# Kernel optimization log

Hardware: AMD Instinct MI355X
Metric: run time of the kernel (lower is better)

The kernel has to match this reference:

```python
import jax, jax.numpy as jnp
import numpy as np

B, T, F, D, O, L = 64, 512, 20, 1024, 1095, 3


def setup_inputs() -> dict:
    key = jax.random.key(0)
    ks = jax.random.split(key, 8)
    return {
        "x": jax.random.normal(ks[0], (B, T, F), jnp.float32),
        "c": jnp.zeros((L, B, D), jnp.float32),  # accepted but ignored, like the torch module
        "W1": jax.random.normal(ks[1], (F, D), jnp.float32) * 0.05,
        "b1": jnp.zeros((D,), jnp.float32),
        "sru_W": jax.random.normal(ks[2], (L, D, 3 * D), jnp.float32) * 0.02,
        "sru_v": jax.random.normal(ks[3], (L, 2, D), jnp.float32) * 0.1,  # v_f, v_r per layer
        "sru_b": jnp.zeros((L, 2, D), jnp.float32),  # b_f, b_r per layer
        "W3": jax.random.normal(ks[4], (D, O), jnp.float32) * 0.02,
        "b3": jnp.zeros((O,), jnp.float32),
    }


def _sru_layer(h, W, vf, vr, bf, br):
    # h: (t, b, d) time-major
    t, b, d = h.shape
    U = jnp.einsum('tbd,de->tbe', h, W).reshape(t, b, 3, d)

    def step(c_prev, inp):
        u0, u1, u2, xt = inp
        f = jax.nn.sigmoid(u1 + vf * c_prev + bf)
        c_new = f * c_prev + (1.0 - f) * u0
        r = jax.nn.sigmoid(u2 + vr * c_new + br)
        h_t = r * c_new + (1.0 - r) * xt  # highway, identity activation (sru default)
        return c_new, h_t

    c0 = jnp.zeros((b, d), h.dtype)
    c_fin, h_out = jax.lax.scan(step, c0, (U[:, :, 0], U[:, :, 1], U[:, :, 2], h))
    return h_out, c_fin


def reference(x, c, W1, b1, sru_W, sru_v, sru_b, W3, b3):
    b, t, f = x.shape
    h = (x.reshape(b * t, f) @ W1 + b1).reshape(b, t, -1)
    h = jnp.transpose(h, (1, 0, 2))  # (t, b, d) time-major
    c_fins = []
    for l in range(L):
        h, c_fin = _sru_layer(h, sru_W[l], sru_v[l, 0], sru_v[l, 1], sru_b[l, 0], sru_b[l, 1])
        c_fins.append(c_fin)
    h = jnp.transpose(h, (1, 0, 2)).reshape(b * t, -1)
    y = h @ W3 + b3  # (b*t, O)
    return y, jnp.stack(c_fins)
```

## Files before the change

### kernel.cpp

```cpp
#include <hip/hip_runtime.h>
#include <hip/hip_bf16.h>

#define B_ 64
#define T_ 512
#define F_ 20
#define D_ 1024
#define O_ 1095
#define L_ 3
#define OPAD 1280

typedef __attribute__((ext_vector_type(8))) short bf16x8;
typedef __attribute__((ext_vector_type(4))) float f32x4;

__device__ __forceinline__ void async16(const void* g, void* l) {
    __builtin_amdgcn_global_load_lds(
        (const __attribute__((address_space(1))) unsigned int*)g,
        (__attribute__((address_space(3))) unsigned int*)l, 16, 0, 0);
}

__global__ __launch_bounds__(256) void fc1_kernel(
    const float* __restrict__ x, const float* __restrict__ W1,
    const float* __restrict__ b1, __hip_bfloat16* __restrict__ h)
{
    __shared__ float xs[64][F_];
    const int tid = threadIdx.x;
    const int d4  = tid * 4;
    const int r0  = blockIdx.x * 64;
    const int t   = r0 >> 6;

    for (int i = tid; i < 64 * F_; i += 256) {
        int r = i / F_, f = i - r * F_;
        xs[r][f] = x[((size_t)r * T_ + t) * F_ + f];
    }

    float4 w[F_];
#pragma unroll
    for (int f = 0; f < F_; ++f)
        w[f] = *(const float4*)(W1 + (size_t)f * D_ + d4);
    float4 bias = *(const float4*)(b1 + d4);

    __syncthreads();

    for (int r = 0; r < 64; ++r) {
        float a0 = bias.x, a1 = bias.y, a2 = bias.z, a3 = bias.w;
#pragma unroll
        for (int f = 0; f < F_; ++f) {
            float xv = xs[r][f];
            a0 = fmaf(xv, w[f].x, a0);
            a1 = fmaf(xv, w[f].y, a1);
            a2 = fmaf(xv, w[f].z, a2);
            a3 = fmaf(xv, w[f].w, a3);
        }
        union { __hip_bfloat162 h2[2]; float2 f2; } o;
        o.h2[0] = __float22bfloat162_rn(float2{a0, a1});
        o.h2[1] = __float22bfloat162_rn(float2{a2, a3});
        *(float2*)(h + ((size_t)(r0 + r) << 10) + d4) = o.f2;
    }
}

__global__ __launch_bounds__(256) void transpose_cast(
    const float* __restrict__ in, __hip_bfloat16* __restrict__ out,
    int K, int N, int Npad)
{
    __shared__ float tile[32][33];
    int k0 = blockIdx.x * 32;
    int n0 = blockIdx.y * 32;
    int tx = threadIdx.x & 31, ty = threadIdx.x >> 5;
#pragma unroll
    for (int r = 0; r < 4; ++r) {
        int n = n0 + tx;
        int k = k0 + ty + r * 8;
        tile[ty + r * 8][tx] = (n < N) ? in[(size_t)k * N + n] : 0.f;
    }
    __syncthreads();
#pragma unroll
    for (int r = 0; r < 4; ++r) {
        int nn = n0 + ty + r * 8;
        out[(size_t)nn * K + k0 + tx] = __float2bfloat16(tile[tx][ty + r * 8]);
    }
}

template<bool GUARD_N, bool REMAP, bool OUT_BF16>
__global__ __launch_bounds__(512, 2) void gemm256(
    const __hip_bfloat16* __restrict__ A,
    const __hip_bfloat16* __restrict__ Bt,
    void* __restrict__ Cv,
    int ldc, int Nreal, const float* __restrict__ bias, int nTilesN)
{
    constexpr int K  = 1024;
    constexpr int NT = K / 64;

    __shared__ __align__(16) char smem[131072];
    char* As = smem;
    char* Bs = smem + 65536;

    const int tid  = threadIdx.x;
    const int lane = tid & 63;
    const int w    = tid >> 6;

    const int nwg = gridDim.x;
    const int q8 = nwg >> 3, r8 = nwg & 7;
    const int xcd = blockIdx.x & 7, loc = blockIdx.x >> 3;
    const int wgid = (xcd < r8 ? xcd * (q8 + 1)
                               : r8 * (q8 + 1) + (xcd - r8) * q8) + loc;
    const int by = wgid / nTilesN;
    const int bx = wgid - by * nTilesN;
    const int tileM = by * 256;
    const int tileN = bx * 256;

    const int wm = (w >> 2) * 128;
    const int wn = (w & 3) * 64;
    const int lr = lane & 15;
    const int kl = lane >> 4;
    const int sw = (lr & 7) << 4;

    const int srow = w * 8 + (lane >> 3);
    const int scol = ((lane & 7) ^ ((lane >> 3) & 7)) << 3;
    const __hip_bfloat16* pAs = A  + (size_t)(tileM + srow) * K + scol;
    const __hip_bfloat16* pBs = Bt + (size_t)(tileN + srow) * K + scol;
    const int ldsW = w * 1024;

    f32x4  acc[8][4] = {};
    bf16x8 a[4][2], b[4][2];

    auto stageA = [&](int kt, int h) {
        char* dst = As + ((kt & 1) << 15) + (h << 14) + ldsW;
        const __hip_bfloat16* src = pAs + (size_t)h * 128 * K + kt * 64;
        async16(src, dst);
        async16(src + 64 * K, dst + 8192);
    };
    auto stageB = [&](int kt, int h) {
        char* dst = Bs + ((kt & 1) << 15) + (h << 14) + ldsW;
        const __hip_bfloat16* src = pBs + (size_t)h * 128 * K + kt * 64;
        async16(src, dst);
        async16(src + 64 * K, dst + 8192);
    };
    auto readA = [&](const char* Ab, int ih) {
#pragma unroll
        for (int ii = 0; ii < 4; ++ii) {
            const char* rp = Ab + (wm + ih * 64 + ii * 16 + lr) * 128;
            a[ii][0] = *(const bf16x8*)(rp + ((kl * 16) ^ sw));
            a[ii][1] = *(const bf16x8*)(rp + ((64 + kl * 16) ^ sw));
        }
    };
    auto readB = [&](const char* Bb, int jh) {
#pragma unroll
        for (int jj = 0; jj < 2; ++jj) {
            const char* rp = Bb + (wn + jh * 32 + jj * 16 + lr) * 128;
            b[jh * 2 + jj][0] = *(const bf16x8*)(rp + ((kl * 16) ^ sw));
            b[jh * 2 + jj][1] = *(const bf16x8*)(rp + ((64 + kl * 16) ^ sw));
        }
    };
    auto quad = [&](int ih, int jh) {
#pragma unroll
        for (int kk = 0; kk < 2; ++kk)
#pragma unroll
            for (int ii = 0; ii < 4; ++ii)
#pragma unroll
                for (int jj = 0; jj < 2; ++jj)
                    acc[ih * 4 + ii][jh * 2 + jj] =
                        __builtin_amdgcn_mfma_f32_16x16x32_bf16(
                            a[ii][kk], b[jh * 2 + jj][kk],
                            acc[ih * 4 + ii][jh * 2 + jj], 0, 0, 0);
    };

    stageB(0, 0); stageB(0, 1);
    stageA(0, 0); stageA(0, 1);
    stageB(1, 0); stageB(1, 1);
    asm volatile("s_waitcnt vmcnt(4)" ::: "memory");
    __builtin_amdgcn_s_barrier();

    for (int t = 0; t < NT; ++t) {
        const char* Ab = As + ((t & 1) << 15);
        const char* Bb = Bs + ((t & 1) << 15);
        readA(Ab, 0);
        readB(Bb, 0);
        if (t + 1 < NT) stageA(t + 1, 0);
        __builtin_amdgcn_s_barrier();
        asm volatile("s_waitcnt lgkmcnt(0)" ::: "memory");
        __builtin_amdgcn_s_setprio(1);
        quad(0, 0);
        __builtin_amdgcn_s_setprio(0);
        __builtin_amdgcn_s_barrier();
        readB(Bb, 1);
        if (t + 1 < NT) stageA(t + 1, 1);
        __builtin_amdgcn_s_barrier();
        asm volatile("s_waitcnt lgkmcnt(0)" ::: "memory");
        __builtin_amdgcn_s_setprio(1);
        quad(0, 1);
        __builtin_amdgcn_s_setprio(0);
        __builtin_amdgcn_s_barrier();
        readA(Ab, 1);
        if (t + 2 < NT) stageB(t + 2, 0);
        __builtin_amdgcn_s_barrier();
        asm volatile("s_waitcnt lgkmcnt(0)" ::: "memory");
        __builtin_amdgcn_s_setprio(1);
        quad(1, 1);
        __builtin_amdgcn_s_setprio(0);
        __builtin_amdgcn_s_barrier();
        if (t + 2 < NT) stageB(t + 2, 1);
        __builtin_amdgcn_s_barrier();
        asm volatile("s_waitcnt lgkmcnt(0)" ::: "memory");
        __builtin_amdgcn_s_setprio(1);
        quad(1, 0);
        __builtin_amdgcn_s_setprio(0);
        if (t + 2 < NT) asm volatile("s_waitcnt vmcnt(4)" ::: "memory");
        else            asm volatile("s_waitcnt vmcnt(0)" ::: "memory");
        __builtin_amdgcn_s_barrier();
    }
    __syncthreads();

    const int rquad = (lane >> 4) * 4;

    if (OUT_BF16) {
        __hip_bfloat16* stg = (__hip_bfloat16*)smem + (size_t)w * 4608;
        __hip_bfloat16* Cb = (__hip_bfloat16*)Cv;
#pragma unroll
        for (int hh = 0; hh < 2; ++hh) {
            if (hh) __syncthreads();
#pragma unroll
            for (int ii = 0; ii < 4; ++ii) {
                int i = hh * 4 + ii;
#pragma unroll
                for (int r = 0; r < 4; ++r) {
                    int row = ii * 16 + rquad + r;
#pragma unroll
                    for (int j = 0; j < 4; ++j)
                        stg[row * 72 + j * 16 + lr] =
                            __float2bfloat16(acc[i][j][r]);
                }
            }
            __syncthreads();
#pragma unroll
            for (int rr = 0; rr < 8; ++rr) {
                int row  = rr * 8 + (lane >> 3);
                int colb = (lane & 7) * 8;
                bf16x8 vd = *(const bf16x8*)(stg + row * 72 + colb);
                int m = tileM + wm + hh * 64 + row;
                int n = tileN + wn + colb;
                size_t orow = REMAP ? ((size_t)(m & (B_ - 1)) * T_ + (m >> 6))
                                    : (size_t)m;
                *(bf16x8*)(Cb + orow * ldc + n) = vd;
            }
        }
    } else {
        float* stgf = (float*)smem + (size_t)w * 2176;
        float* Cf = (float*)Cv;
#pragma unroll
        for (int p = 0; p < 4; ++p) {
            if (p) __syncthreads();
#pragma unroll
            for (int ii = 0; ii < 2; ++ii) {
                int i = p * 2 + ii;
#pragma unroll
                for (int r = 0; r < 4; ++r) {
                    int row = ii * 16 + rquad + r;
#pragma unroll
                    for (int j = 0; j < 4; ++j) {
                        int n = tileN + wn + j * 16 + lr;
                        float v = acc[i][j][r];
                        if (bias && (!GUARD_N || n < Nreal)) v += bias[n];
                        stgf[row * 68 + j * 16 + lr] = v;
                    }
                }
            }
            __syncthreads();
            for (int row = 0; row < 32; ++row) {
                float vd = stgf[row * 68 + lane];
                int m = tileM + wm + p * 32 + row;
                int n = tileN + wn + lane;
                size_t orow = REMAP ? ((size_t)(m & (B_ - 1)) * T_ + (m >> 6))
                                    : (size_t)m;
                if (!GUARD_N || n < Nreal) Cf[orow * ldc + n] = vd;
            }
        }
    }
}

__global__ __launch_bounds__(256) void sru_scan(
    const __hip_bfloat16* __restrict__ U, __hip_bfloat16* __restrict__ h,
    const float* __restrict__ v, const float* __restrict__ bvec,
    float* __restrict__ carry, float* __restrict__ cfin,
    int t0, int t1)
{
    constexpr int G = 16;
    int idx = blockIdx.x * 256 + threadIdx.x;
    int d = idx & (D_ - 1);
    int b = idx >> 10;

    float vf = v[d],      vr = v[D_ + d];
    float bf = bvec[d],   br = bvec[D_ + d];
    float c = (t0 == 0) ? 0.f : carry[idx];

    const size_t su = (size_t)B_ * 3 * D_;
    const size_t sh = (size_t)B_ * D_;
    const __hip_bfloat16* Up = U + (size_t)b * (3 * D_) + d;
    __hip_bfloat16* hp = h + (size_t)t0 * sh + idx;

    const int nsteps  = t1 - t0;
    const int ngroups = nsteps / G;

    float a0[G], a1[G], a2[G], ax[G];
    float b0[G], b1v[G], b2[G], bx[G];

    auto load_into = [&](int g, float (&u0)[G], float (&u1)[G],
                         float (&u2)[G], float (&xt)[G]) {
        const __hip_bfloat16* Upn = Up + (size_t)g * G * su;
        const __hip_bfloat16* hpn = hp + (size_t)g * G * sh;
#pragma unroll
        for (int j = 0; j < G; ++j) {
            u0[j] = __bfloat162float(Upn[0]);
            u1[j] = __bfloat162float(Upn[D_]);
            u2[j] = __bfloat162float(Upn[2 * D_]);
            xt[j] = __bfloat162float(*hpn);
            Upn += su; hpn += sh;
        }
    };
    auto compute = [&](int g, const float (&u0)[G], const float (&u1)[G],
                       const float (&u2)[G], const float (&xt)[G]) {
        __hip_bfloat16* hps = hp + (size_t)g * G * sh;
#pragma unroll
        for (int j = 0; j < G; ++j) {
            float f = 1.f / (1.f + __expf(-(u1[j] + vf * c + bf)));
            c = f * c + (1.f - f) * u0[j];
            float r = 1.f / (1.f + __expf(-(u2[j] + vr * c + br)));
            *hps = __float2bfloat16(r * c + (1.f - r) * xt[j]);
            hps += sh;
        }
    };

    if (ngroups > 0) {
        load_into(0, a0, a1, a2, ax);
        int g = 0;
        for (; g + 2 <= ngroups; g += 2) {
            load_into(g + 1, b0, b1v, b2, bx);
            compute(g, a0, a1, a2, ax);
            if (g + 2 < ngroups) load_into(g + 2, a0, a1, a2, ax);
            compute(g + 1, b0, b1v, b2, bx);
        }
        if (g < ngroups) compute(g, a0, a1, a2, ax);
    }
    for (int t = ngroups * G; t < nsteps; ++t) {
        const __hip_bfloat16* Upn = Up + (size_t)t * su;
        float u0 = __bfloat162float(Upn[0]);
        float u1 = __bfloat162float(Upn[D_]);
        float u2 = __bfloat162float(Upn[2 * D_]);
        __hip_bfloat16* hps = hp + (size_t)t * sh;
        float xv = __bfloat162float(*hps);
        float f = 1.f / (1.f + __expf(-(u1 + vf * c + bf)));
        c = f * c + (1.f - f) * u0;
        float r = 1.f / (1.f + __expf(-(u2 + vr * c + br)));
        *hps = __float2bfloat16(r * c + (1.f - r) * xv);
    }

    carry[idx] = c;
    if (cfin) cfin[idx] = c;
}

extern "C" void kernel_launch(void* const* d_in, const int* in_sizes, int n_in,
                              void* d_out, int out_size, void* d_ws, size_t ws_size,
                              hipStream_t stream)
{
    const float* x     = (const float*)d_in[0];
    const float* W1    = (const float*)d_in[2];
    const float* b1    = (const float*)d_in[3];
    const float* sru_W = (const float*)d_in[4];
    const float* sru_v = (const float*)d_in[5];
    const float* sru_b = (const float*)d_in[6];
    const float* W3    = (const float*)d_in[7];
    const float* b3    = (const float*)d_in[8];

    float* y    = (float*)d_out;
    float* cfin = y + (size_t)(B_ * T_) * O_;

    char* ws = (char*)d_ws;
    size_t off = 0;
    __hip_bfloat16* h = (__hip_bfloat16*)(ws + off);
    off += (size_t)T_ * B_ * D_ * sizeof(__hip_bfloat16);
    float* carry = (float*)(ws + off);
    off += (size_t)B_ * D_ * sizeof(float);
    __hip_bfloat16* Wt = (__hip_bfloat16*)(ws + off);
    off += (size_t)L_ * 3 * D_ * D_ * sizeof(__hip_bfloat16);
    __hip_bfloat16* Wt3 = (__hip_bfloat16*)(ws + off);
    off += (size_t)OPAD * D_ * sizeof(__hip_bfloat16);
    __hip_bfloat16* Ubuf = (__hip_bfloat16*)(ws + off);

    size_t perT  = (size_t)B_ * 3 * D_ * sizeof(__hip_bfloat16);
    size_t avail = (ws_size > off) ? ws_size - off : 0;
    int chunkT = (int)(avail / perT);
    if (chunkT > 128) chunkT = 128;
    chunkT &= ~15;
    if (chunkT < 16) chunkT = 16;

    for (int l = 0; l < L_; ++l) {
        dim3 gt(D_ / 32, (3 * D_) / 32);
        transpose_cast<<<gt, 256, 0, stream>>>(
            sru_W + (size_t)l * D_ * 3 * D_, Wt + (size_t)l * 3 * D_ * D_,
            D_, 3 * D_, 3 * D_);
    }
    {
        dim3 gt(D_ / 32, OPAD / 32);
        transpose_cast<<<gt, 256, 0, stream>>>(W3, Wt3, D_, O_, OPAD);
    }

    fc1_kernel<<<(T_ * B_) / 64, 256, 0, stream>>>(x, W1, b1, h);

    for (int l = 0; l < L_; ++l) {
        const __hip_bfloat16* Wl = Wt + (size_t)l * 3 * D_ * D_;
        const float* vl = sru_v + (size_t)l * 2 * D_;
        const float* bl = sru_b + (size_t)l * 2 * D_;
        for (int t0 = 0; t0 < T_; t0 += chunkT) {
            int t1 = (t0 + chunkT > T_) ? T_ : (t0 + chunkT);
            int rows = (t1 - t0) * B_;
            int nTilesN = (3 * D_) / 256;
            int nblocks = (rows / 256) * nTilesN;
            gemm256<false, false, true><<<nblocks, 512, 0, stream>>>(
                h + (size_t)t0 * B_ * D_, Wl, Ubuf,
                3 * D_, 3 * D_, nullptr, nTilesN);
            sru_scan<<<(B_ * D_) / 256, 256, 0, stream>>>(
                Ubuf, h, vl, bl, carry,
                (t1 == T_) ? (cfin + (size_t)l * B_ * D_) : nullptr,
                t0, t1);
        }
    }

    {
        int nTilesN = OPAD / 256;
        int nblocks = ((B_ * T_) / 256) * nTilesN;
        gemm256<true, true, false><<<nblocks, 512, 0, stream>>>(
            h, Wt3, y, O_, O_, b3, nTilesN);
    }
}
```

Measured before the change: 1.338 ms.

## Make GEMM persistent with next-tile prefetch overlapping epilogue, enlarge scan chunk

Turns the 256x256 GEMM into a persistent kernel whose grid is capped at 256 workgroups, each looping over tiles. While the current tile finishes, it prefetches the first K-slices of the next tile into LDS so the epilogue overlaps with loads. The epilogue now stages through a separate LDS region without block-wide syncs, and the time chunk per GEMM/scan pair grows to 256 steps, halving launches per layer. This adds LDS aliasing complexity and grid-stride scheduling that may load-balance worse.

```diff
diff --git a/kernel.cpp b/kernel.cpp
--- a/kernel.cpp
+++ b/kernel.cpp
@@ -85,28 +85,27 @@
     const __hip_bfloat16* __restrict__ A,
     const __hip_bfloat16* __restrict__ Bt,
     void* __restrict__ Cv,
-    int ldc, int Nreal, const float* __restrict__ bias, int nTilesN)
+    int ldc, int Nreal, const float* __restrict__ bias,
+    int nTilesN, int nTiles)
 {
     constexpr int K  = 1024;
     constexpr int NT = K / 64;
 
     __shared__ __align__(16) char smem[131072];
-    char* As = smem;
-    char* Bs = smem + 65536;
+    char* As  = smem;
+    char* Bs  = smem + 65536;
+    char* rep = smem + 32768;
 
     const int tid  = threadIdx.x;
     const int lane = tid & 63;
     const int w    = tid >> 6;
 
-    const int nwg = gridDim.x;
-    const int q8 = nwg >> 3, r8 = nwg & 7;
+    const int G  = gridDim.x;
+    const int q8 = G >> 3, r8 = G & 7;
     const int xcd = blockIdx.x & 7, loc = blockIdx.x >> 3;
     const int wgid = (xcd < r8 ? xcd * (q8 + 1)
                                : r8 * (q8 + 1) + (xcd - r8) * q8) + loc;
-    const int by = wgid / nTilesN;
-    const int bx = wgid - by * nTilesN;
-    const int tileM = by * 256;
-    const int tileN = bx * 256;
+    if (wgid >= nTiles) return;
 
     const int wm = (w >> 2) * 128;
     const int wn = (w & 3) * 64;
@@ -116,22 +115,26 @@
 
     const int srow = w * 8 + (lane >> 3);
     const int scol = ((lane & 7) ^ ((lane >> 3) & 7)) << 3;
-    const __hip_bfloat16* pAs = A  + (size_t)(tileM + srow) * K + scol;
-    const __hip_bfloat16* pBs = Bt + (size_t)(tileN + srow) * K + scol;
     const int ldsW = w * 1024;
 
-    f32x4  acc[8][4] = {};
+    int tile = wgid;
+    int by = tile / nTilesN, bx = tile - by * nTilesN;
+    int tM = by * 256, tN = bx * 256;
+    const __hip_bfloat16* pA = A  + (size_t)(tM + srow) * K + scol;
+    const __hip_bfloat16* pB = Bt + (size_t)(tN + srow) * K + scol;
+
+    f32x4  acc[8][4];
     bf16x8 a[4][2], b[4][2];
 
-    auto stageA = [&](int kt, int h) {
-        char* dst = As + ((kt & 1) << 15) + (h << 14) + ldsW;
-        const __hip_bfloat16* src = pAs + (size_t)h * 128 * K + kt * 64;
+    auto stA = [&](const __hip_bfloat16* base, int kk, int h, int buf) {
+        char* dst = As + (buf << 15) + (h << 14) + ldsW;
+        const __hip_bfloat16* src = base + (size_t)h * 128 * K + kk * 64;
         async16(src, dst);
         async16(src + 64 * K, dst + 8192);
     };
-    auto stageB = [&](int kt, int h) {
-        char* dst = Bs + ((kt & 1) << 15) + (h << 14) + ldsW;
-        const __hip_bfloat16* src = pBs + (size_t)h * 128 * K + kt * 64;
+    auto stB = [&](const __hip_bfloat16* base, int kk, int h, int buf) {
+        char* dst = Bs + (buf << 15) + (h << 14) + ldsW;
+        const __hip_bfloat16* src = base + (size_t)h * 128 * K + kk * 64;
         async16(src, dst);
         async16(src + 64 * K, dst + 8192);
     };
@@ -164,116 +167,129 @@
                             acc[ih * 4 + ii][jh * 2 + jj], 0, 0, 0);
     };
 
-    stageB(0, 0); stageB(0, 1);
-    stageA(0, 0); stageA(0, 1);
-    stageB(1, 0); stageB(1, 1);
+    stB(pB, 0, 0, 0); stB(pB, 0, 1, 0);
+    stA(pA, 0, 0, 0); stA(pA, 0, 1, 0);
+    stB(pB, 1, 0, 1); stB(pB, 1, 1, 1);
     asm volatile("s_waitcnt vmcnt(4)" ::: "memory");
     __builtin_amdgcn_s_barrier();
 
-    for (int t = 0; t < NT; ++t) {
-        const char* Ab = As + ((t & 1) << 15);
-        const char* Bb = Bs + ((t & 1) << 15);
-        readA(Ab, 0);
-        readB(Bb, 0);
-        if (t + 1 < NT) stageA(t + 1, 0);
-        __builtin_amdgcn_s_barrier();
-        asm volatile("s_waitcnt lgkmcnt(0)" ::: "memory");
-        __builtin_amdgcn_s_setprio(1);
-        quad(0, 0);
-        __builtin_amdgcn_s_setprio(0);
-        __builtin_amdgcn_s_barrier();
-        readB(Bb, 1);
-        if (t + 1 < NT) stageA(t + 1, 1);
-        __builtin_amdgcn_s_barrier();
-        asm volatile("s_waitcnt lgkmcnt(0)" ::: "memory");
-        __builtin_amdgcn_s_setprio(1);
-        quad(0, 1);
-        __builtin_amdgcn_s_setprio(0);
-        __builtin_amdgcn_s_barrier();
-        readA(Ab, 1);
-        if (t + 2 < NT) stageB(t + 2, 0);
-        __builtin_amdgcn_s_barrier();
-        asm volatile("s_waitcnt lgkmcnt(0)" ::: "memory");
-        __builtin_amdgcn_s_setprio(1);
-        quad(1, 1);
-        __builtin_amdgcn_s_setprio(0);
-        __builtin_amdgcn_s_barrier();
-        if (t + 2 < NT) stageB(t + 2, 1);
-        __builtin_amdgcn_s_barrier();
-        asm volatile("s_waitcnt lgkmcnt(0)" ::: "memory");
-        __builtin_amdgcn_s_setprio(1);
-        quad(1, 0);
-        __builtin_amdgcn_s_setprio(0);
-        if (t + 2 < NT) asm volatile("s_waitcnt vmcnt(4)" ::: "memory");
-        else            asm volatile("s_waitcnt vmcnt(0)" ::: "memory");
-        __builtin_amdgcn_s_barrier();
-    }
-    __syncthreads();
-
-    const int rquad = (lane >> 4) * 4;
-
-    if (OUT_BF16) {
-        __hip_bfloat16* stg = (__hip_bfloat16*)smem + (size_t)w * 4608;
-        __hip_bfloat16* Cb = (__hip_bfloat16*)Cv;
-#pragma unroll
-        for (int hh = 0; hh < 2; ++hh) {
-            if (hh) __syncthreads();
-#pragma unroll
-            for (int ii = 0; ii < 4; ++ii) {
-                int i = hh * 4 + ii;
-#pragma unroll
-                for (int r = 0; r < 4; ++r) {
-                    int row = ii * 16 + rquad + r;
-#pragma unroll
-                    for (int j = 0; j < 4; ++j)
-                        stg[row * 72 + j * 16 + lr] =
-                            __float2bfloat16(acc[i][j][r]);
+    for (;;) {
+        const bool hasNext = (tile + G) < nTiles;
+        int tMn = 0, tNn = 0;
+        const __hip_bfloat16 *pAn = A, *pBn = Bt;
+        if (hasNext) {
+            int t2 = tile + G;
+            int byn = t2 / nTilesN, bxn = t2 - byn * nTilesN;
+            tMn = byn * 256; tNn = bxn * 256;
+            pAn = A  + (size_t)(tMn + srow) * K + scol;
+            pBn = Bt + (size_t)(tNn + srow) * K + scol;
+        }
+#pragma unroll
+        for (int i = 0; i < 8; ++i)
+#pragma unroll
+            for (int j = 0; j < 4; ++j)
+                acc[i][j] = f32x4{0.f, 0.f, 0.f, 0.f};
+
+        for (int t = 0; t < NT; ++t) {
+            const char* Ab = As + ((t & 1) << 15);
+            const char* Bb = Bs + ((t & 1) << 15);
+            readA(Ab, 0);
+            readB(Bb, 0);
+            if (t + 1 < NT)      stA(pA,  t + 1, 0, (t + 1) & 1);
+            else if (hasNext)    stA(pAn, 0,     0, 0);
+            __builtin_amdgcn_s_barrier();
+            asm volatile("s_waitcnt lgkmcnt(0)" ::: "memory");
+            __builtin_amdgcn_s_setprio(1);
+            quad(0, 0);
+            __builtin_amdgcn_s_setprio(0);
+            __builtin_amdgcn_s_barrier();
+            readB(Bb, 1);
+            if (t + 1 < NT)      stA(pA,  t + 1, 1, (t + 1) & 1);
+            else if (hasNext)    stA(pAn, 0,     1, 0);
+            __builtin_amdgcn_s_barrier();
+            asm volatile("s_waitcnt lgkmcnt(0)" ::: "memory");
+            __builtin_amdgcn_s_setprio(1);
+            quad(0, 1);
+            __builtin_amdgcn_s_setprio(0);
+            __builtin_amdgcn_s_barrier();
+            readA(Ab, 1);
+            if (t + 2 < NT)      stB(pB,  t + 2,      0, t & 1);
+            else if (hasNext)    stB(pBn, t + 2 - NT, 0, t & 1);
+            __builtin_amdgcn_s_barrier();
+            asm volatile("s_waitcnt lgkmcnt(0)" ::: "memory");
+            __builtin_amdgcn_s_setprio(1);
+            quad(1, 1);
+            __builtin_amdgcn_s_setprio(0);
+            __builtin_amdgcn_s_barrier();
+            if (t + 2 < NT)      stB(pB,  t + 2,      1, t & 1);
+            else if (hasNext)    stB(pBn, t + 2 - NT, 1, t & 1);
+            __builtin_amdgcn_s_barrier();
+            asm volatile("s_waitcnt lgkmcnt(0)" ::: "memory");
+            __builtin_amdgcn_s_setprio(1);
+            quad(1, 0);
+            __builtin_amdgcn_s_setprio(0);
+            if (t + 2 < NT || hasNext) asm volatile("s_waitcnt vmcnt(4)" ::: "memory");
+            else                       asm volatile("s_waitcnt vmcnt(0)" ::: "memory");
+            __builtin_amdgcn_s_barrier();
+        }
+
+        const int rquad = (lane >> 4) * 4;
+
+        if (OUT_BF16) {
+            __hip_bfloat16* stg = (__hip_bfloat16*)rep + w * 2048;
+            __hip_bfloat16* Cb = (__hip_bfloat16*)Cv;
+#pragma unroll
+            for (int p = 0; p < 4; ++p) {
+#pragma unroll
+                for (int ii = 0; ii < 2; ++ii) {
+                    int i = p * 2 + ii;
+#pragma unroll
+                    for (int r = 0; r < 4; ++r)
+#pragma unroll
+                        for (int j = 0; j < 4; ++j)
+                            stg[(ii * 16 + rquad + r) * 64 + j * 16 + lr] =
+                                __float2bfloat16(acc[i][j][r]);
+                }
+#pragma unroll
+                for (int rr = 0; rr < 4; ++rr) {
+                    int row  = rr * 8 + (lane >> 3);
+                    int colb = (lane & 7) * 8;
+                    bf16x8 vd = *(const bf16x8*)(stg + row * 64 + colb);
+                    int m = tM + wm + p * 32 + row;
+                    int n = tN + wn + colb;
+                    size_t orow = REMAP ? ((size_t)(m & (B_ - 1)) * T_ + (m >> 6))
+                                        : (size_t)m;
+                    *(bf16x8*)(Cb + orow * ldc + n) = vd;
                 }
             }
-            __syncthreads();
-#pragma unroll
-            for (int rr = 0; rr < 8; ++rr) {
-                int row  = rr * 8 + (lane >> 3);
-                int colb = (lane & 7) * 8;
-                bf16x8 vd = *(const bf16x8*)(stg + row * 72 + colb);
-                int m = tileM + wm + hh * 64 + row;
-                int n = tileN + wn + colb;
-                size_t orow = REMAP ? ((size_t)(m & (B_ - 1)) * T_ + (m >> 6))
-                                    : (size_t)m;
-                *(bf16x8*)(Cb + orow * ldc + n) = vd;
-            }
-        }
-    } else {
-        float* stgf = (float*)smem + (size_t)w * 2176;
-        float* Cf = (float*)Cv;
-#pragma unroll
-        for (int p = 0; p < 4; ++p) {
-            if (p) __syncthreads();
-#pragma unroll
-            for (int ii = 0; ii < 2; ++ii) {
-                int i = p * 2 + ii;
-#pragma unroll
-                for (int r = 0; r < 4; ++r) {
-                    int row = ii * 16 + rquad + r;
+        } else {
+            float* stgf = (float*)rep + w * 1024;
+            float* Cf = (float*)Cv;
+#pragma unroll
+            for (int i = 0; i < 8; ++i) {
+#pragma unroll
+                for (int r = 0; r < 4; ++r)
 #pragma unroll
                     for (int j = 0; j < 4; ++j) {
-                        int n = tileN + wn + j * 16 + lr;
+                        int n = tN + wn + j * 16 + lr;
                         float v = acc[i][j][r];
                         if (bias && (!GUARD_N || n < Nreal)) v += bias[n];
-                        stgf[row * 68 + j * 16 + lr] = v;
+                        stgf[(rquad + r) * 64 + j * 16 + lr] = v;
                     }
+                for (int row = 0; row < 16; ++row) {
+                    float vd = stgf[row * 64 + lane];
+                    int m = tM + wm + i * 16 + row;
+                    int n = tN + wn + lane;
+                    size_t orow = REMAP ? ((size_t)(m & (B_ - 1)) * T_ + (m >> 6))
+                                        : (size_t)m;
+                    if (!GUARD_N || n < Nreal) Cf[orow * ldc + n] = vd;
                 }
             }
-            __syncthreads();
-            for (int row = 0; row < 32; ++row) {
-                float vd = stgf[row * 68 + lane];
-                int m = tileM + wm + p * 32 + row;
-                int n = tileN + wn + lane;
-                size_t orow = REMAP ? ((size_t)(m & (B_ - 1)) * T_ + (m >> 6))
-                                    : (size_t)m;
-                if (!GUARD_N || n < Nreal) Cf[orow * ldc + n] = vd;
-            }
-        }
+        }
+
+        if (!hasNext) break;
+        tile += G; tM = tMn; tN = tNn; pA = pAn; pB = pBn;
+        __syncthreads();
     }
 }
 
@@ -388,7 +404,7 @@
     size_t perT  = (size_t)B_ * 3 * D_ * sizeof(__hip_bfloat16);
     size_t avail = (ws_size > off) ? ws_size - off : 0;
     int chunkT = (int)(avail / perT);
-    if (chunkT > 128) chunkT = 128;
+    if (chunkT > 256) chunkT = 256;
     chunkT &= ~15;
     if (chunkT < 16) chunkT = 16;
 
@@ -413,10 +429,11 @@
             int t1 = (t0 + chunkT > T_) ? T_ : (t0 + chunkT);
             int rows = (t1 - t0) * B_;
             int nTilesN = (3 * D_) / 256;
-            int nblocks = (rows / 256) * nTilesN;
-            gemm256<false, false, true><<<nblocks, 512, 0, stream>>>(
+            int nTiles  = (rows / 256) * nTilesN;
+            int grid    = nTiles < 256 ? nTiles : 256;
+            gemm256<false, false, true><<<grid, 512, 0, stream>>>(
                 h + (size_t)t0 * B_ * D_, Wl, Ubuf,
-                3 * D_, 3 * D_, nullptr, nTilesN);
+                3 * D_, 3 * D_, nullptr, nTilesN, nTiles);
             sru_scan<<<(B_ * D_) / 256, 256, 0, stream>>>(
                 Ubuf, h, vl, bl, carry,
                 (t1 == T_) ? (cfin + (size_t)l * B_ * D_) : nullptr,
@@ -426,8 +443,8 @@
 
     {
         int nTilesN = OPAD / 256;
-        int nblocks = ((B_ * T_) / 256) * nTilesN;
-        gemm256<true, true, false><<<nblocks, 512, 0, stream>>>(
-            h, Wt3, y, O_, O_, b3, nTilesN);
-    }
-}
+        int nTiles  = ((B_ * T_) / 256) * nTilesN;
+        gemm256<true, true, false><<<256, 512, 0, stream>>>(
+            h, Wt3, y, O_, O_, b3, nTilesN, nTiles);
+    }
+}
```

Result: faster. 1.121 ms (-16.3%).
